# Kernel tuning notes

Hardware: AMD Instinct MI355X
Metric: run time of the kernel (lower is better)

## Reference

```python
import jax, jax.numpy as jnp
import numpy as np

NUM_SONGS = 2000
N1 = NUM_SONGS + 1  # incl. padding idx 0
EMB = 64
B = 32
S = 5    # num_prev_shows
M = 25   # max_songs_per_show


def setup_inputs() -> dict:
    key = jax.random.key(0)
    ks = jax.random.split(key, 32)
    def lin(k, i, o):
        kw, kb = jax.random.split(k)
        s = 1.0 / np.sqrt(i)
        return (jax.random.uniform(kw, (i, o), jnp.float32, -s, s),
                jax.random.uniform(kb, (o,), jnp.float32, -s, s))
    song_emb = jax.random.normal(ks[0], (N1, EMB), jnp.float32)
    song_emb = song_emb.at[0].set(0.0)  # padding_idx=0
    gcn_w1, gcn_b1 = lin(ks[1], EMB, EMB)
    gcn_w2, gcn_b2 = lin(ks[2], EMB, EMB)
    q_w, q_b = lin(ks[3], EMB, EMB)
    k_w, k_b = lin(ks[4], EMB, EMB)
    v_w, v_b = lin(ks[5], EMB, EMB)
    venue_t = jax.random.normal(ks[6], (200, EMB // 4), jnp.float32)
    tour_t = jax.random.normal(ks[7], (20, EMB // 4), jnp.float32)
    country_t = jax.random.normal(ks[8], (50, EMB // 8), jnp.float32)
    fest_t = jax.random.normal(ks[9], (2, EMB // 8), jnp.float32)
    mara_t = jax.random.normal(ks[10], (2, EMB // 8), jnp.float32)
    ctx_in = EMB // 2 + 3 * (EMB // 8)  # 56
    ctx_w, ctx_b = lin(ks[11], ctx_in, EMB)
    p1_w, p1_b = lin(ks[12], EMB * 3, EMB * 2)
    p2_w, p2_b = lin(ks[13], EMB * 2, EMB)
    p3_w, p3_b = lin(ks[14], EMB, 1)
    return {
        'song_ids': jax.random.randint(ks[20], (B,), 0, N1),
        'prev_setlists': jax.random.randint(ks[21], (B, S, M), 0, N1),
        'venue_ids': jax.random.randint(ks[22], (B,), 0, 200),
        'tour_ids': jax.random.randint(ks[23], (B,), 0, 20),
        'country_ids': jax.random.randint(ks[24], (B,), 0, 50),
        'is_festival': jax.random.randint(ks[25], (B,), 0, 2),
        'is_marathon': jax.random.randint(ks[26], (B,), 0, 2),
        'song_emb': song_emb,
        'gcn_w1': gcn_w1, 'gcn_b1': gcn_b1, 'gcn_w2': gcn_w2, 'gcn_b2': gcn_b2,
        'q_w': q_w, 'q_b': q_b, 'k_w': k_w, 'k_b': k_b, 'v_w': v_w, 'v_b': v_b,
        'venue_t': venue_t, 'tour_t': tour_t, 'country_t': country_t,
        'fest_t': fest_t, 'mara_t': mara_t,
        'ctx_w': ctx_w, 'ctx_b': ctx_b,
        'p1_w': p1_w, 'p1_b': p1_b, 'p2_w': p2_w, 'p2_b': p2_b,
        'p3_w': p3_w, 'p3_b': p3_b,
    }


def _build_adj(prev_setlists):
    # co-occurrence counts via one scatter-add (replaces nested python loops)
    b, s, m = prev_setlists.shape
    mask = prev_setlists > 0
    pair_ok = (mask[:, :, :, None] & mask[:, :, None, :]
               & ~jnp.eye(m, dtype=bool))  # exclude same position i==j
    flat_idx = (prev_setlists[:, :, :, None] * N1
                + prev_setlists[:, :, None, :]).reshape(b, -1)
    w = pair_ok.astype(jnp.float32).reshape(b, -1)
    adj = jnp.zeros((b, N1 * N1), jnp.float32)
    adj = adj.at[jnp.arange(b)[:, None], flat_idx].add(w)
    adj = adj.reshape(b, N1, N1)
    return adj / (adj.sum(axis=2, keepdims=True) + 1e-10)


def _forward(song_ids, prev_setlists, venue_ids, tour_ids, country_ids,
             is_festival, is_marathon, song_emb, gcn_w1, gcn_b1, gcn_w2,
             gcn_b2, q_w, q_b, k_w, k_b, v_w, v_b, venue_t, tour_t,
             country_t, fest_t, mara_t, ctx_w, ctx_b, p1_w, p1_b, p2_w,
             p2_b, p3_w, p3_b):
    b = song_ids.shape[0]
    adj = _build_adj(prev_setlists)                      # [B,N1,N1]
    x = jnp.broadcast_to(song_emb[None], (b, N1, EMB))   # [B,N1,E]
    for w_, b_ in ((gcn_w1, gcn_b1), (gcn_w2, gcn_b2)):
        agg = jnp.einsum('bnm,bme->bne', adj, x)
        x = jax.nn.relu(agg @ w_ + b_)
    song_embs = x
    # ragged masked-mean show embeddings
    mask = (prev_setlists > 0).astype(jnp.float32)       # [B,S,M]
    gathered = jax.vmap(lambda se, ids: se[ids])(song_embs, prev_setlists)  # [B,S,M,E]
    cnt = mask.sum(-1, keepdims=True)                    # [B,S,1]
    show_embs = jnp.where(cnt > 0,
                          (gathered * mask[..., None]).sum(2) / jnp.maximum(cnt, 1.0),
                          0.0)                           # [B,S,E]
    ctx = jnp.concatenate([venue_t[venue_ids], tour_t[tour_ids],
                           country_t[country_ids], fest_t[is_festival],
                           mara_t[is_marathon]], axis=-1)
    ctx = ctx @ ctx_w + ctx_b                            # [B,E]
    # temporal attention
    q = ctx @ q_w + q_b                                  # [B,E]
    k = show_embs @ k_w + k_b                            # [B,S,E]
    v = show_embs @ v_w + v_b
    scores = jnp.einsum('be,bse->bs', q, k) / jnp.sqrt(jnp.float32(EMB))
    attn = jax.nn.softmax(scores, axis=-1)
    attended = jnp.einsum('bs,bse->be', attn, v)
    cand = song_embs[jnp.arange(b), song_ids]
    h = jnp.concatenate([cand, ctx, attended], axis=-1)  # [B,3E]
    h = jax.nn.relu(h @ p1_w + p1_b)   # dropout is eval-mode identity
    h = jax.nn.relu(h @ p2_w + p2_b)
    logits = (h @ p3_w + p3_b).squeeze(-1)
    return jax.nn.sigmoid(logits)


def reference(song_ids, prev_setlists, venue_ids, tour_ids, country_ids,
              is_festival, is_marathon, song_emb, gcn_w1, gcn_b1, gcn_w2,
              gcn_b2, q_w, q_b, k_w, k_b, v_w, v_b, venue_t, tour_t,
              country_t, fest_t, mara_t, ctx_w, ctx_b, p1_w, p1_b, p2_w,
              p2_b, p3_w, p3_b):
    return _forward(song_ids, prev_setlists, venue_ids, tour_ids,
                    country_ids, is_festival, is_marathon, song_emb,
                    gcn_w1, gcn_b1, gcn_w2, gcn_b2, q_w, q_b, k_w, k_b,
                    v_w, v_b, venue_t, tour_t, country_t, fest_t, mara_t,
                    ctx_w, ctx_b, p1_w, p1_b, p2_w, p2_b, p3_w, p3_b)
```

## Files before the change

### kernel.cpp

```cpp
#include <hip/hip_runtime.h>

#define N1    2001
#define EMB   64
#define NSHOW 5
#define MSONG 25
#define NPOS  (NSHOW * MSONG)
#define MAXU  128
#define NT    1024
#define WT    68

__global__ __launch_bounds__(NT)
__attribute__((amdgpu_waves_per_eu(4, 4)))
void setsgnn_kernel(
    const int* __restrict__ song_ids,
    const int* __restrict__ prev_setlists,
    const int* __restrict__ venue_ids,
    const int* __restrict__ tour_ids,
    const int* __restrict__ country_ids,
    const int* __restrict__ is_festival,
    const int* __restrict__ is_marathon,
    const float* __restrict__ song_emb,
    const float* __restrict__ gcn_w1, const float* __restrict__ gcn_b1,
    const float* __restrict__ gcn_w2, const float* __restrict__ gcn_b2,
    const float* __restrict__ q_w,  const float* __restrict__ q_b,
    const float* __restrict__ k_w,  const float* __restrict__ k_b,
    const float* __restrict__ v_w,  const float* __restrict__ v_b,
    const float* __restrict__ venue_t, const float* __restrict__ tour_t,
    const float* __restrict__ country_t, const float* __restrict__ fest_t,
    const float* __restrict__ mara_t,
    const float* __restrict__ ctx_w, const float* __restrict__ ctx_b,
    const float* __restrict__ p1_w,  const float* __restrict__ p1_b,
    const float* __restrict__ p2_w,  const float* __restrict__ p2_b,
    const float* __restrict__ p3_w,  const float* __restrict__ p3_b,
    float* __restrict__ out)
{
    const int b    = blockIdx.x;
    const int tid  = threadIdx.x;
    const int wv   = tid >> 6;
    const int lane = tid & 63;
    const int col0 = tid & 63;
    const int eq0  = tid >> 6;

    __shared__ __align__(16) float xb0[MAXU][EMB];
    __shared__ __align__(16) float wldsT[2][EMB][WT];
    __shared__ __align__(16) float ctxw_l[56][EMB];
    __shared__ __align__(16) float qw_l[EMB][EMB];
    __shared__ __align__(16) float blds[2][EMB];
    __shared__ __align__(16) float bias_ctx[EMB], bias_q[EMB], bias_k[EMB], bias_v[EMB];
    __shared__ __align__(16) float bias_p1[128], bias_p2[EMB], bias_p3w[EMB];
    __shared__ float bias_p3b;
    __shared__ unsigned short idmap[N1];
    __shared__ int   sl[NPOS];
    __shared__ int   pmap[NPOS];
    __shared__ int   list_ids[MAXU];
    __shared__ float c_us[MAXU][NSHOW];
    __shared__ float occv[MAXU];
    __shared__ float invv[MAXU];
    __shared__ float cntm1[NSHOW];
    __shared__ float invc[NSHOW];
    __shared__ int   U_cnt;
    __shared__ __align__(16) float Xsum[NSHOW][EMB];
    __shared__ float XW[NSHOW][EMB];
    __shared__ float ctxin[56];
    __shared__ float ctxv[EMB];
    __shared__ float qv[EMB];
    __shared__ float vatt[NSHOW][EMB];
    __shared__ float attnw[NSHOW];
    __shared__ float hbuf[3 * EMB];
    __shared__ float h1b[128];
    __shared__ float partial[NT];

    float w1r[4], w2r[4];
    #pragma unroll
    for (int j = 0; j < 4; j++) w1r[j] = gcn_w1[(eq0 * 4 + j) * EMB + col0];
    #pragma unroll
    for (int j = 0; j < 4; j++) w2r[j] = gcn_w2[(eq0 * 4 + j) * EMB + col0];
    const float4 qw4 = ((const float4*)q_w)[tid];
    float4 cw4 = make_float4(0.f, 0.f, 0.f, 0.f);
    if (tid < 896) cw4 = ((const float4*)ctx_w)[tid];
    float4 bb;
    if (tid < 32) bb = (tid < 16) ? ((const float4*)gcn_b1)[tid]
                                  : ((const float4*)gcn_b2)[tid - 16];
    const int slr = (tid < NPOS) ? prev_setlists[b * NPOS + tid] : 0;
    const int sid    = song_ids[b];
    const int vid    = venue_ids[b];
    const int tourid = tour_ids[b];
    const int cid    = country_ids[b];
    const int fid    = is_festival[b];
    const int mid    = is_marathon[b];

    for (int i = tid; i < N1; i += NT) idmap[i] = 0xFFFFu;
    if (tid < MAXU * NSHOW) ((float*)c_us)[tid] = 0.f;
    if (tid < NPOS) sl[tid] = slr;
    if (tid == 0) U_cnt = 0;
    *(float4*)&wldsT[0][col0][eq0 * 4] = make_float4(w1r[0], w1r[1], w1r[2], w1r[3]);
    *(float4*)&wldsT[1][col0][eq0 * 4] = make_float4(w2r[0], w2r[1], w2r[2], w2r[3]);
    ((float4*)qw_l)[tid] = qw4;
    if (tid < 896) ((float4*)ctxw_l)[tid] = cw4;
    if (tid < 32) ((float4*)blds)[tid] = bb;
    {
        int r = tid - 256;
        if (r >= 0 && r < 16)        ((float4*)bias_ctx)[r]       = ((const float4*)ctx_b)[r];
        else if (r >= 16 && r < 32)  ((float4*)bias_q)[r - 16]    = ((const float4*)q_b)[r - 16];
        else if (r >= 32 && r < 48)  ((float4*)bias_k)[r - 32]    = ((const float4*)k_b)[r - 32];
        else if (r >= 48 && r < 64)  ((float4*)bias_v)[r - 48]    = ((const float4*)v_b)[r - 48];
        else if (r >= 64 && r < 96)  ((float4*)bias_p1)[r - 64]   = ((const float4*)p1_b)[r - 64];
        else if (r >= 96 && r < 112) ((float4*)bias_p2)[r - 96]   = ((const float4*)p2_b)[r - 96];
        else if (r >= 112 && r < 128)((float4*)bias_p3w)[r - 112] = ((const float4*)p3_w)[r - 112];
        else if (r == 128)           bias_p3b = p3_b[0];
    }
    __syncthreads();

    if (tid < NPOS) { int id = sl[tid]; if (id > 0) idmap[id] = 1u; }
    if (tid == NPOS) idmap[sid] = 1u;
    if (tid >= 128 && tid < 128 + NSHOW) {
        int s = tid - 128, c = 0;
        for (int i = 0; i < MSONG; i++) c += (sl[s * MSONG + i] > 0) ? 1 : 0;
        cntm1[s] = (float)(c - 1);
        invc[s] = 1.f / fmaxf((float)c, 1.f);
    }
    if (tid >= 144 && tid < 200) {
        int e = tid - 144; float val;
        if (e < 16)      val = venue_t[vid * 16 + e];
        else if (e < 32) val = tour_t[tourid * 16 + (e - 16)];
        else if (e < 40) val = country_t[cid * 8 + (e - 32)];
        else if (e < 48) val = fest_t[fid * 8 + (e - 40)];
        else             val = mara_t[mid * 8 + (e - 48)];
        ctxin[e] = val;
    }
    __syncthreads();

    for (int i = tid; i < N1; i += NT) {
        const bool p = (idmap[i] == 1u);
        const unsigned long long m = __ballot(p);
        int base = 0;
        if (lane == 0) { int c = __popcll(m); if (c) base = atomicAdd(&U_cnt, c); }
        base = __shfl(base, 0, 64);
        if (p) {
            int r = __popcll(m & ((1ull << lane) - 1ull));
            int u = base + r;
            idmap[i] = (unsigned short)u;
            list_ids[u] = i;
        }
    }
    __syncthreads();
    const int U = U_cnt;

    if (tid < NPOS) {
        int id = sl[tid];
        int pm = (id > 0) ? (int)idmap[id] : -1;
        pmap[tid] = pm;
        if (pm >= 0) atomicAdd(&c_us[pm][tid / MSONG], 1.f);
    }
    if (tid >= 896 && tid < 960) {
        int c = tid - 896;
        float acc = bias_ctx[c];
        #pragma unroll
        for (int e = 0; e < 56; e++) acc += ctxin[e] * ctxw_l[e][c];
        ctxv[c] = acc;
    }
    for (int t = tid; t < MAXU * (EMB / 4); t += NT) {
        int u = t >> 4, e4 = t & 15;
        float4 v = make_float4(0.f, 0.f, 0.f, 0.f);
        if (u < U) v = ((const float4*)(song_emb + list_ids[u] * EMB))[e4];
        *(float4*)&xb0[u][e4 * 4] = v;
    }
    __syncthreads();

    if (tid < MAXU) {
        float o = 0.f, r = 0.f;
        #pragma unroll
        for (int s = 0; s < NSHOW; s++) { float cc = c_us[tid][s]; o += cc; r += cc * cntm1[s]; }
        occv[tid] = o; invv[tid] = 1.f / (r + 1e-10f);
    }
    if (tid >= 128 && tid < 192) {
        int c = tid - 128;
        float acc = bias_q[c];
        #pragma unroll
        for (int e = 0; e < EMB; e++) acc += ctxv[e] * qw_l[e][c];
        qv[c] = acc;
    }
    if (wv >= 6 && wv < 11) {
        int s = wv - 6;
        int pm[MSONG];
        #pragma unroll
        for (int i = 0; i < MSONG; i++) pm[i] = pmap[s * MSONG + i];
        float acc = 0.f;
        #pragma unroll
        for (int i = 0; i < MSONG; i++) if (pm[i] >= 0) acc += xb0[pm[i]][lane];
        Xsum[s][lane] = acc;
    }
    __syncthreads();

    if (tid < NSHOW * EMB) {
        int s = tid >> 6, c = tid & 63;
        float acc = 0.f;
        #pragma unroll 4
        for (int e4 = 0; e4 < 16; e4++) {
            const float4 w4 = *(const float4*)&wldsT[0][c][e4 * 4];
            const float4 xs = *(const float4*)&Xsum[s][e4 * 4];
            acc += w4.x * xs.x + w4.y * xs.y + w4.z * xs.z + w4.w * xs.w;
        }
        XW[s][c] = acc;
    }
    __syncthreads();

    #define GCN_BODY(L)                                                          \
    {                                                                            \
        const float bias = blds[L][lane];                                        \
        float y[8];                                                              \
        _Pragma("unroll")                                                        \
        for (int uu = 0; uu < 8; ++uu) y[uu] = 0.f;                              \
        _Pragma("unroll 4")                                                      \
        for (int e4 = 0; e4 < 16; ++e4) {                                        \
            float4 a[8];                                                         \
            _Pragma("unroll")                                                    \
            for (int uu = 0; uu < 8; ++uu)                                       \
                a[uu] = *(const float4*)&xb0[(uu << 4) | wv][e4 * 4];            \
            const float4 w4 = *(const float4*)&wldsT[L][lane][e4 * 4];           \
            _Pragma("unroll")                                                    \
            for (int uu = 0; uu < 8; ++uu)                                       \
                y[uu] += a[uu].x * w4.x + a[uu].y * w4.y                         \
                       + a[uu].z * w4.z + a[uu].w * w4.w;                        \
        }                                                                        \
        _Pragma("unroll")                                                        \
        for (int uu = 0; uu < 8; ++uu) {                                         \
            const int u = (uu << 4) | wv;                                        \
            float acc = c_us[u][0] * XW[0][lane] + c_us[u][1] * XW[1][lane]      \
                      + c_us[u][2] * XW[2][lane] + c_us[u][3] * XW[3][lane]      \
                      + c_us[u][4] * XW[4][lane];                                \
            float val = (acc - occv[u] * y[uu]) * invv[u] + bias;                \
            xb0[u][lane] = fmaxf(val, 0.f);                                      \
        }                                                                        \
    }

    GCN_BODY(0)
    __syncthreads();

    {
        float kr[4];
        #pragma unroll
        for (int j = 0; j < 4; j++) kr[j] = k_w[(eq0 * 4 + j) * EMB + col0];
        if (wv >= 6 && wv < 11) {
            int s = wv - 6;
            int pm[MSONG];
            #pragma unroll
            for (int i = 0; i < MSONG; i++) pm[i] = pmap[s * MSONG + i];
            float acc = 0.f;
            #pragma unroll
            for (int i = 0; i < MSONG; i++) if (pm[i] >= 0) acc += xb0[pm[i]][lane];
            Xsum[s][lane] = acc;
        }
        *(float4*)&wldsT[0][col0][eq0 * 4] = make_float4(kr[0], kr[1], kr[2], kr[3]);
    }
    __syncthreads();

    if (tid < NSHOW * EMB) {
        int s = tid >> 6, c = tid & 63;
        float acc = 0.f;
        #pragma unroll 4
        for (int e4 = 0; e4 < 16; e4++) {
            const float4 w4 = *(const float4*)&wldsT[1][c][e4 * 4];
            const float4 xs = *(const float4*)&Xsum[s][e4 * 4];
            acc += w4.x * xs.x + w4.y * xs.y + w4.z * xs.z + w4.w * xs.w;
        }
        XW[s][c] = acc;
    }
    __syncthreads();

    float vr[4];
    #pragma unroll
    for (int j = 0; j < 4; j++) vr[j] = v_w[(eq0 * 4 + j) * EMB + col0];
    GCN_BODY(1)
    __syncthreads();

    *(float4*)&wldsT[1][col0][eq0 * 4] = make_float4(vr[0], vr[1], vr[2], vr[3]);
    const int kk1 = tid >> 7, o1 = tid & 127;
    const int kk2 = tid >> 6, o2 = lane;
    float p1wr[24], p2wr[8];
    #pragma unroll
    for (int j = 0; j < 24; j++) p1wr[j] = p1_w[(kk1 * 24 + j) * 128 + o1];
    #pragma unroll
    for (int j = 0; j < 8; j++)  p2wr[j] = p2_w[(kk2 * 8 + j) * 64 + o2];

    if (wv >= 6 && wv < 11) {
        int s = wv - 6;
        int pm[MSONG];
        #pragma unroll
        for (int i = 0; i < MSONG; i++) pm[i] = pmap[s * MSONG + i];
        float acc = 0.f;
        #pragma unroll
        for (int i = 0; i < MSONG; i++) if (pm[i] >= 0) acc += xb0[pm[i]][lane];
        Xsum[s][lane] = acc;
    }
    if (tid < 64)                    hbuf[tid] = xb0[(int)idmap[sid]][tid];
    else if (tid >= 64 && tid < 128) hbuf[tid] = ctxv[tid - 64];
    __syncthreads();

    if (wv < NSHOW) {
        float s0 = 0.f;
        #pragma unroll 4
        for (int e4 = 0; e4 < 16; e4++) {
            const float4 w4 = *(const float4*)&wldsT[0][lane][e4 * 4];
            const float4 xs = *(const float4*)&Xsum[wv][e4 * 4];
            s0 += w4.x * xs.x + w4.y * xs.y + w4.z * xs.z + w4.w * xs.w;
        }
        float kk = s0 * invc[wv] + bias_k[lane];
        float p = kk * qv[lane];
        #pragma unroll
        for (int o = 32; o > 0; o >>= 1) p += __shfl_xor(p, o, 64);
        if (lane == 0) attnw[wv] = p * 0.125f;
    }
    if (wv >= 5 && wv < 10) {
        int s = wv - 5;
        float s0 = 0.f;
        #pragma unroll 4
        for (int e4 = 0; e4 < 16; e4++) {
            const float4 w4 = *(const float4*)&wldsT[1][lane][e4 * 4];
            const float4 xs = *(const float4*)&Xsum[s][e4 * 4];
            s0 += w4.x * xs.x + w4.y * xs.y + w4.z * xs.z + w4.w * xs.w;
        }
        vatt[s][lane] = s0 * invc[s] + bias_v[lane];
    }
    __syncthreads();

    if (wv == 0) {
        float a0 = attnw[0], a1 = attnw[1], a2 = attnw[2], a3 = attnw[3], a4 = attnw[4];
        float mx = fmaxf(fmaxf(fmaxf(a0, a1), fmaxf(a2, a3)), a4);
        float e0 = expf(a0 - mx), e1 = expf(a1 - mx), e2 = expf(a2 - mx),
              e3 = expf(a3 - mx), e4 = expf(a4 - mx);
        float isum = 1.f / (e0 + e1 + e2 + e3 + e4);
        float att = (e0 * vatt[0][lane] + e1 * vatt[1][lane] + e2 * vatt[2][lane]
                   + e3 * vatt[3][lane] + e4 * vatt[4][lane]) * isum;
        hbuf[2 * EMB + lane] = att;
    }
    __syncthreads();

    {
        float acc = (kk1 == 0) ? bias_p1[o1] : 0.f;
        #pragma unroll
        for (int j = 0; j < 24; j++) acc += hbuf[kk1 * 24 + j] * p1wr[j];
        partial[tid] = acc;
    }
    __syncthreads();

    if (tid < 128) {
        float acc = 0.f;
        #pragma unroll
        for (int kk = 0; kk < 8; kk++) acc += partial[kk * 128 + tid];
        h1b[tid] = fmaxf(acc, 0.f);
    }
    __syncthreads();

    {
        float acc = (kk2 == 0) ? bias_p2[o2] : 0.f;
        #pragma unroll
        for (int j = 0; j < 8; j++) acc += h1b[kk2 * 8 + j] * p2wr[j];
        partial[tid] = acc;
    }
    __syncthreads();

    if (wv == 0) {
        float acc = 0.f;
        #pragma unroll
        for (int kk = 0; kk < 16; kk++) acc += partial[kk * 64 + lane];
        float h2 = fmaxf(acc, 0.f);
        float p = h2 * bias_p3w[lane];
        #pragma unroll
        for (int o = 32; o > 0; o >>= 1) p += __shfl_xor(p, o, 64);
        if (lane == 0) out[b] = 1.f / (1.f + expf(-(p + bias_p3b)));
    }
}

extern "C" void kernel_launch(void* const* d_in, const int* in_sizes, int n_in,
                              void* d_out, int out_size, void* d_ws, size_t ws_size,
                              hipStream_t stream) {
    (void)n_in; (void)out_size; (void)d_ws; (void)ws_size;
    const int B = in_sizes[0];
    setsgnn_kernel<<<B, NT, 0, stream>>>(
        (const int*)d_in[0], (const int*)d_in[1], (const int*)d_in[2],
        (const int*)d_in[3], (const int*)d_in[4], (const int*)d_in[5],
        (const int*)d_in[6],
        (const float*)d_in[7],
        (const float*)d_in[8],  (const float*)d_in[9],
        (const float*)d_in[10], (const float*)d_in[11],
        (const float*)d_in[12], (const float*)d_in[13],
        (const float*)d_in[14], (const float*)d_in[15],
        (const float*)d_in[16], (const float*)d_in[17],
        (const float*)d_in[18], (const float*)d_in[19],
        (const float*)d_in[20], (const float*)d_in[21],
        (const float*)d_in[22],
        (const float*)d_in[23], (const float*)d_in[24],
        (const float*)d_in[25], (const float*)d_in[26],
        (const float*)d_in[27], (const float*)d_in[28],
        (const float*)d_in[29], (const float*)d_in[30],
        (float*)d_out);
}
```

Baseline: 32.73 us.

## Reassociate GCN aggregation to sum transformed rows and fuse attention into MLP

```diff
diff --git a/kernel.cpp b/kernel.cpp
--- a/kernel.cpp
+++ b/kernel.cpp
@@ -42,6 +42,7 @@
     const int eq0  = tid >> 6;
 
     __shared__ __align__(16) float xb0[MAXU][EMB];
+    __shared__ __align__(16) float ybuf[MAXU][EMB];
     __shared__ __align__(16) float wldsT[2][EMB][WT];
     __shared__ __align__(16) float ctxw_l[56][EMB];
     __shared__ __align__(16) float qw_l[EMB][EMB];
@@ -66,7 +67,6 @@
     __shared__ float qv[EMB];
     __shared__ float vatt[NSHOW][EMB];
     __shared__ float attnw[NSHOW];
-    __shared__ float hbuf[3 * EMB];
     __shared__ float h1b[128];
     __shared__ float partial[NT];
 
@@ -143,15 +143,6 @@
             list_ids[u] = i;
         }
     }
-    __syncthreads();
-    const int U = U_cnt;
-
-    if (tid < NPOS) {
-        int id = sl[tid];
-        int pm = (id > 0) ? (int)idmap[id] : -1;
-        pmap[tid] = pm;
-        if (pm >= 0) atomicAdd(&c_us[pm][tid / MSONG], 1.f);
-    }
     if (tid >= 896 && tid < 960) {
         int c = tid - 896;
         float acc = bias_ctx[c];
@@ -159,56 +150,11 @@
         for (int e = 0; e < 56; e++) acc += ctxin[e] * ctxw_l[e][c];
         ctxv[c] = acc;
     }
-    for (int t = tid; t < MAXU * (EMB / 4); t += NT) {
-        int u = t >> 4, e4 = t & 15;
-        float4 v = make_float4(0.f, 0.f, 0.f, 0.f);
-        if (u < U) v = ((const float4*)(song_emb + list_ids[u] * EMB))[e4];
-        *(float4*)&xb0[u][e4 * 4] = v;
-    }
-    __syncthreads();
-
-    if (tid < MAXU) {
-        float o = 0.f, r = 0.f;
-        #pragma unroll
-        for (int s = 0; s < NSHOW; s++) { float cc = c_us[tid][s]; o += cc; r += cc * cntm1[s]; }
-        occv[tid] = o; invv[tid] = 1.f / (r + 1e-10f);
-    }
-    if (tid >= 128 && tid < 192) {
-        int c = tid - 128;
-        float acc = bias_q[c];
-        #pragma unroll
-        for (int e = 0; e < EMB; e++) acc += ctxv[e] * qw_l[e][c];
-        qv[c] = acc;
-    }
-    if (wv >= 6 && wv < 11) {
-        int s = wv - 6;
-        int pm[MSONG];
-        #pragma unroll
-        for (int i = 0; i < MSONG; i++) pm[i] = pmap[s * MSONG + i];
-        float acc = 0.f;
-        #pragma unroll
-        for (int i = 0; i < MSONG; i++) if (pm[i] >= 0) acc += xb0[pm[i]][lane];
-        Xsum[s][lane] = acc;
-    }
-    __syncthreads();
-
-    if (tid < NSHOW * EMB) {
-        int s = tid >> 6, c = tid & 63;
-        float acc = 0.f;
-        #pragma unroll 4
-        for (int e4 = 0; e4 < 16; e4++) {
-            const float4 w4 = *(const float4*)&wldsT[0][c][e4 * 4];
-            const float4 xs = *(const float4*)&Xsum[s][e4 * 4];
-            acc += w4.x * xs.x + w4.y * xs.y + w4.z * xs.z + w4.w * xs.w;
-        }
-        XW[s][c] = acc;
-    }
-    __syncthreads();
-
-    #define GCN_BODY(L)                                                          \
+    __syncthreads();
+    const int U = U_cnt;
+
+    #define Y_COMPUTE(L)                                                         \
     {                                                                            \
-        const float bias = blds[L][lane];                                        \
-        float y[8];                                                              \
         _Pragma("unroll")                                                        \
         for (int uu = 0; uu < 8; ++uu) y[uu] = 0.f;                              \
         _Pragma("unroll 4")                                                      \
@@ -224,6 +170,12 @@
                        + a[uu].z * w4.z + a[uu].w * w4.w;                        \
         }                                                                        \
         _Pragma("unroll")                                                        \
+        for (int uu = 0; uu < 8; ++uu) ybuf[(uu << 4) | wv][lane] = y[uu];       \
+    }
+    #define COMBINE(L)                                                           \
+    {                                                                            \
+        const float bias = blds[L][lane];                                        \
+        _Pragma("unroll")                                                        \
         for (int uu = 0; uu < 8; ++uu) {                                         \
             const int u = (uu << 4) | wv;                                        \
             float acc = c_us[u][0] * XW[0][lane] + c_us[u][1] * XW[1][lane]      \
@@ -234,47 +186,75 @@
         }                                                                        \
     }
 
-    GCN_BODY(0)
+    float y[8];
+    if (tid < NPOS) {
+        int id = sl[tid];
+        int pm = (id > 0) ? (int)idmap[id] : -1;
+        pmap[tid] = pm;
+        if (pm >= 0) atomicAdd(&c_us[pm][tid / MSONG], 1.f);
+    }
+    if (tid >= 128 && tid < 192) {
+        int c = tid - 128;
+        float acc = bias_q[c];
+        #pragma unroll
+        for (int e = 0; e < EMB; e++) acc += ctxv[e] * qw_l[e][c];
+        qv[c] = acc;
+    }
+    #pragma unroll
+    for (int g = 0; g < 2; ++g) {
+        const int uu = g * 4 + (lane >> 4);
+        const int u  = (uu << 4) | wv;
+        const int e4 = lane & 15;
+        float4 v = make_float4(0.f, 0.f, 0.f, 0.f);
+        if (u < U) v = ((const float4*)(song_emb + list_ids[u] * EMB))[e4];
+        *(float4*)&xb0[u][e4 * 4] = v;
+    }
+    Y_COMPUTE(0)
     __syncthreads();
 
     {
         float kr[4];
         #pragma unroll
         for (int j = 0; j < 4; j++) kr[j] = k_w[(eq0 * 4 + j) * EMB + col0];
-        if (wv >= 6 && wv < 11) {
-            int s = wv - 6;
-            int pm[MSONG];
-            #pragma unroll
-            for (int i = 0; i < MSONG; i++) pm[i] = pmap[s * MSONG + i];
+        if (wv < NSHOW) {
             float acc = 0.f;
             #pragma unroll
-            for (int i = 0; i < MSONG; i++) if (pm[i] >= 0) acc += xb0[pm[i]][lane];
-            Xsum[s][lane] = acc;
+            for (int i = 0; i < MSONG; i++) {
+                int pm = pmap[wv * MSONG + i];
+                if (pm >= 0) acc += ybuf[pm][lane];
+            }
+            XW[wv][lane] = acc;
+        }
+        if (tid >= 320 && tid < 448) {
+            int u = tid - 320;
+            float o = 0.f, r = 0.f;
+            #pragma unroll
+            for (int s = 0; s < NSHOW; s++) { float cc = c_us[u][s]; o += cc; r += cc * cntm1[s]; }
+            occv[u] = o; invv[u] = 1.f / (r + 1e-10f);
         }
         *(float4*)&wldsT[0][col0][eq0 * 4] = make_float4(kr[0], kr[1], kr[2], kr[3]);
     }
     __syncthreads();
 
-    if (tid < NSHOW * EMB) {
-        int s = tid >> 6, c = tid & 63;
+    float vr[4];
+    #pragma unroll
+    for (int j = 0; j < 4; j++) vr[j] = v_w[(eq0 * 4 + j) * EMB + col0];
+    COMBINE(0)
+    Y_COMPUTE(1)
+    __syncthreads();
+
+    if (wv < NSHOW) {
         float acc = 0.f;
-        #pragma unroll 4
-        for (int e4 = 0; e4 < 16; e4++) {
-            const float4 w4 = *(const float4*)&wldsT[1][c][e4 * 4];
-            const float4 xs = *(const float4*)&Xsum[s][e4 * 4];
-            acc += w4.x * xs.x + w4.y * xs.y + w4.z * xs.z + w4.w * xs.w;
-        }
-        XW[s][c] = acc;
-    }
-    __syncthreads();
-
-    float vr[4];
-    #pragma unroll
-    for (int j = 0; j < 4; j++) vr[j] = v_w[(eq0 * 4 + j) * EMB + col0];
-    GCN_BODY(1)
-    __syncthreads();
-
+        #pragma unroll
+        for (int i = 0; i < MSONG; i++) {
+            int pm = pmap[wv * MSONG + i];
+            if (pm >= 0) acc += ybuf[pm][lane];
+        }
+        XW[wv][lane] = acc;
+    }
     *(float4*)&wldsT[1][col0][eq0 * 4] = make_float4(vr[0], vr[1], vr[2], vr[3]);
+    __syncthreads();
+
     const int kk1 = tid >> 7, o1 = tid & 127;
     const int kk2 = tid >> 6, o2 = lane;
     float p1wr[24], p2wr[8];
@@ -282,6 +262,8 @@
     for (int j = 0; j < 24; j++) p1wr[j] = p1_w[(kk1 * 24 + j) * 128 + o1];
     #pragma unroll
     for (int j = 0; j < 8; j++)  p2wr[j] = p2_w[(kk2 * 8 + j) * 64 + o2];
+    COMBINE(1)
+    __syncthreads();
 
     if (wv >= 6 && wv < 11) {
         int s = wv - 6;
@@ -293,8 +275,6 @@
         for (int i = 0; i < MSONG; i++) if (pm[i] >= 0) acc += xb0[pm[i]][lane];
         Xsum[s][lane] = acc;
     }
-    if (tid < 64)                    hbuf[tid] = xb0[(int)idmap[sid]][tid];
-    else if (tid >= 64 && tid < 128) hbuf[tid] = ctxv[tid - 64];
     __syncthreads();
 
     if (wv < NSHOW) {
@@ -324,22 +304,27 @@
     }
     __syncthreads();
 
-    if (wv == 0) {
+    {
         float a0 = attnw[0], a1 = attnw[1], a2 = attnw[2], a3 = attnw[3], a4 = attnw[4];
         float mx = fmaxf(fmaxf(fmaxf(a0, a1), fmaxf(a2, a3)), a4);
-        float e0 = expf(a0 - mx), e1 = expf(a1 - mx), e2 = expf(a2 - mx),
-              e3 = expf(a3 - mx), e4 = expf(a4 - mx);
-        float isum = 1.f / (e0 + e1 + e2 + e3 + e4);
-        float att = (e0 * vatt[0][lane] + e1 * vatt[1][lane] + e2 * vatt[2][lane]
-                   + e3 * vatt[3][lane] + e4 * vatt[4][lane]) * isum;
-        hbuf[2 * EMB + lane] = att;
-    }
-    __syncthreads();
-
-    {
+        float ex0 = expf(a0 - mx), ex1 = expf(a1 - mx), ex2 = expf(a2 - mx),
+              ex3 = expf(a3 - mx), ex4 = expf(a4 - mx);
+        float isum = 1.f / (ex0 + ex1 + ex2 + ex3 + ex4);
+        const int uc = (int)idmap[sid];
         float acc = (kk1 == 0) ? bias_p1[o1] : 0.f;
         #pragma unroll
-        for (int j = 0; j < 24; j++) acc += hbuf[kk1 * 24 + j] * p1wr[j];
+        for (int j = 0; j < 24; j++) {
+            int e = kk1 * 24 + j;
+            float h;
+            if (e < 64)       h = xb0[uc][e];
+            else if (e < 128) h = ctxv[e - 64];
+            else {
+                int d = e - 128;
+                h = (ex0 * vatt[0][d] + ex1 * vatt[1][d] + ex2 * vatt[2][d]
+                   + ex3 * vatt[3][d] + ex4 * vatt[4][d]) * isum;
+            }
+            acc += h * p1wr[j];
+        }
         partial[tid] = acc;
     }
     __syncthreads();
```

Result: slower. 35.07 us (+7.2%).

## Preload all four 64x64 weights into LDS upfront and loop the GCN layers

Applied to the files above, without the earlier changes.

```diff
diff --git a/kernel.cpp b/kernel.cpp
--- a/kernel.cpp
+++ b/kernel.cpp
@@ -42,7 +42,7 @@
     const int eq0  = tid >> 6;
 
     __shared__ __align__(16) float xb0[MAXU][EMB];
-    __shared__ __align__(16) float wldsT[2][EMB][WT];
+    __shared__ __align__(16) float wldsT[4][EMB][WT];
     __shared__ __align__(16) float ctxw_l[56][EMB];
     __shared__ __align__(16) float qw_l[EMB][EMB];
     __shared__ __align__(16) float blds[2][EMB];
@@ -70,17 +70,23 @@
     __shared__ float h1b[128];
     __shared__ float partial[NT];
 
-    float w1r[4], w2r[4];
-    #pragma unroll
-    for (int j = 0; j < 4; j++) w1r[j] = gcn_w1[(eq0 * 4 + j) * EMB + col0];
-    #pragma unroll
-    for (int j = 0; j < 4; j++) w2r[j] = gcn_w2[(eq0 * 4 + j) * EMB + col0];
-    const float4 qw4 = ((const float4*)q_w)[tid];
-    float4 cw4 = make_float4(0.f, 0.f, 0.f, 0.f);
-    if (tid < 896) cw4 = ((const float4*)ctx_w)[tid];
-    float4 bb;
-    if (tid < 32) bb = (tid < 16) ? ((const float4*)gcn_b1)[tid]
-                                  : ((const float4*)gcn_b2)[tid - 16];
+    {
+        const float* wps[4] = { gcn_w1, gcn_w2, k_w, v_w };
+        float wr[4][4];
+        #pragma unroll
+        for (int m = 0; m < 4; m++)
+            #pragma unroll
+            for (int j = 0; j < 4; j++) wr[m][j] = wps[m][(eq0 * 4 + j) * EMB + col0];
+        #pragma unroll
+        for (int m = 0; m < 4; m++)
+            *(float4*)&wldsT[m][col0][eq0 * 4] = make_float4(wr[m][0], wr[m][1], wr[m][2], wr[m][3]);
+    }
+    ((float4*)qw_l)[tid] = ((const float4*)q_w)[tid];
+    if (tid < 896) ((float4*)ctxw_l)[tid] = ((const float4*)ctx_w)[tid];
+    if (tid < 32) {
+        float4 bb = (tid < 16) ? ((const float4*)gcn_b1)[tid] : ((const float4*)gcn_b2)[tid - 16];
+        ((float4*)blds)[tid] = bb;
+    }
     const int slr = (tid < NPOS) ? prev_setlists[b * NPOS + tid] : 0;
     const int sid    = song_ids[b];
     const int vid    = venue_ids[b];
@@ -93,11 +99,6 @@
     if (tid < MAXU * NSHOW) ((float*)c_us)[tid] = 0.f;
     if (tid < NPOS) sl[tid] = slr;
     if (tid == 0) U_cnt = 0;
-    *(float4*)&wldsT[0][col0][eq0 * 4] = make_float4(w1r[0], w1r[1], w1r[2], w1r[3]);
-    *(float4*)&wldsT[1][col0][eq0 * 4] = make_float4(w2r[0], w2r[1], w2r[2], w2r[3]);
-    ((float4*)qw_l)[tid] = qw4;
-    if (tid < 896) ((float4*)ctxw_l)[tid] = cw4;
-    if (tid < 32) ((float4*)blds)[tid] = bb;
     {
         int r = tid - 256;
         if (r >= 0 && r < 16)        ((float4*)bias_ctx)[r]       = ((const float4*)ctx_b)[r];
@@ -155,7 +156,7 @@
     if (tid >= 896 && tid < 960) {
         int c = tid - 896;
         float acc = bias_ctx[c];
-        #pragma unroll
+        #pragma unroll 2
         for (int e = 0; e < 56; e++) acc += ctxin[e] * ctxw_l[e][c];
         ctxv[c] = acc;
     }
@@ -176,105 +177,70 @@
     if (tid >= 128 && tid < 192) {
         int c = tid - 128;
         float acc = bias_q[c];
-        #pragma unroll
+        #pragma unroll 2
         for (int e = 0; e < EMB; e++) acc += ctxv[e] * qw_l[e][c];
         qv[c] = acc;
     }
     if (wv >= 6 && wv < 11) {
         int s = wv - 6;
-        int pm[MSONG];
-        #pragma unroll
-        for (int i = 0; i < MSONG; i++) pm[i] = pmap[s * MSONG + i];
         float acc = 0.f;
         #pragma unroll
-        for (int i = 0; i < MSONG; i++) if (pm[i] >= 0) acc += xb0[pm[i]][lane];
+        for (int i = 0; i < MSONG; i++) { int pm = pmap[s * MSONG + i]; if (pm >= 0) acc += xb0[pm][lane]; }
         Xsum[s][lane] = acc;
     }
     __syncthreads();
 
-    if (tid < NSHOW * EMB) {
-        int s = tid >> 6, c = tid & 63;
-        float acc = 0.f;
-        #pragma unroll 4
-        for (int e4 = 0; e4 < 16; e4++) {
-            const float4 w4 = *(const float4*)&wldsT[0][c][e4 * 4];
-            const float4 xs = *(const float4*)&Xsum[s][e4 * 4];
-            acc += w4.x * xs.x + w4.y * xs.y + w4.z * xs.z + w4.w * xs.w;
-        }
-        XW[s][c] = acc;
-    }
-    __syncthreads();
-
-    #define GCN_BODY(L)                                                          \
-    {                                                                            \
-        const float bias = blds[L][lane];                                        \
-        float y[8];                                                              \
-        _Pragma("unroll")                                                        \
-        for (int uu = 0; uu < 8; ++uu) y[uu] = 0.f;                              \
-        _Pragma("unroll 4")                                                      \
-        for (int e4 = 0; e4 < 16; ++e4) {                                        \
-            float4 a[8];                                                         \
-            _Pragma("unroll")                                                    \
-            for (int uu = 0; uu < 8; ++uu)                                       \
-                a[uu] = *(const float4*)&xb0[(uu << 4) | wv][e4 * 4];            \
-            const float4 w4 = *(const float4*)&wldsT[L][lane][e4 * 4];           \
-            _Pragma("unroll")                                                    \
-            for (int uu = 0; uu < 8; ++uu)                                       \
-                y[uu] += a[uu].x * w4.x + a[uu].y * w4.y                         \
-                       + a[uu].z * w4.z + a[uu].w * w4.w;                        \
-        }                                                                        \
-        _Pragma("unroll")                                                        \
-        for (int uu = 0; uu < 8; ++uu) {                                         \
-            const int u = (uu << 4) | wv;                                        \
-            float acc = c_us[u][0] * XW[0][lane] + c_us[u][1] * XW[1][lane]      \
-                      + c_us[u][2] * XW[2][lane] + c_us[u][3] * XW[3][lane]      \
-                      + c_us[u][4] * XW[4][lane];                                \
-            float val = (acc - occv[u] * y[uu]) * invv[u] + bias;                \
-            xb0[u][lane] = fmaxf(val, 0.f);                                      \
-        }                                                                        \
-    }
-
-    GCN_BODY(0)
-    __syncthreads();
-
-    {
-        float kr[4];
-        #pragma unroll
-        for (int j = 0; j < 4; j++) kr[j] = k_w[(eq0 * 4 + j) * EMB + col0];
+    for (int l = 0; l < 2; ++l) {
+        if (wv < NSHOW) {
+            float acc = 0.f;
+            #pragma unroll 2
+            for (int e4 = 0; e4 < 16; e4++) {
+                const float4 w4 = *(const float4*)&wldsT[l][lane][e4 * 4];
+                const float4 xs = *(const float4*)&Xsum[wv][e4 * 4];
+                acc += w4.x * xs.x + w4.y * xs.y + w4.z * xs.z + w4.w * xs.w;
+            }
+            XW[wv][lane] = acc;
+        }
+        __syncthreads();
+
+        {
+            const float bias = blds[l][lane];
+            float y[8];
+            #pragma unroll
+            for (int uu = 0; uu < 8; ++uu) y[uu] = 0.f;
+            #pragma unroll 2
+            for (int e4 = 0; e4 < 16; ++e4) {
+                float4 a[8];
+                #pragma unroll
+                for (int uu = 0; uu < 8; ++uu)
+                    a[uu] = *(const float4*)&xb0[(uu << 4) | wv][e4 * 4];
+                const float4 w4 = *(const float4*)&wldsT[l][lane][e4 * 4];
+                #pragma unroll
+                for (int uu = 0; uu < 8; ++uu)
+                    y[uu] += a[uu].x * w4.x + a[uu].y * w4.y + a[uu].z * w4.z + a[uu].w * w4.w;
+            }
+            #pragma unroll
+            for (int uu = 0; uu < 8; ++uu) {
+                const int u = (uu << 4) | wv;
+                float acc = c_us[u][0] * XW[0][lane] + c_us[u][1] * XW[1][lane]
+                          + c_us[u][2] * XW[2][lane] + c_us[u][3] * XW[3][lane]
+                          + c_us[u][4] * XW[4][lane];
+                float val = (acc - occv[u] * y[uu]) * invv[u] + bias;
+                xb0[u][lane] = fmaxf(val, 0.f);
+            }
+        }
+        __syncthreads();
+
         if (wv >= 6 && wv < 11) {
             int s = wv - 6;
-            int pm[MSONG];
-            #pragma unroll
-            for (int i = 0; i < MSONG; i++) pm[i] = pmap[s * MSONG + i];
             float acc = 0.f;
             #pragma unroll
-            for (int i = 0; i < MSONG; i++) if (pm[i] >= 0) acc += xb0[pm[i]][lane];
+            for (int i = 0; i < MSONG; i++) { int pm = pmap[s * MSONG + i]; if (pm >= 0) acc += xb0[pm][lane]; }
             Xsum[s][lane] = acc;
         }
-        *(float4*)&wldsT[0][col0][eq0 * 4] = make_float4(kr[0], kr[1], kr[2], kr[3]);
-    }
-    __syncthreads();
-
-    if (tid < NSHOW * EMB) {
-        int s = tid >> 6, c = tid & 63;
-        float acc = 0.f;
-        #pragma unroll 4
-        for (int e4 = 0; e4 < 16; e4++) {
-            const float4 w4 = *(const float4*)&wldsT[1][c][e4 * 4];
-            const float4 xs = *(const float4*)&Xsum[s][e4 * 4];
-            acc += w4.x * xs.x + w4.y * xs.y + w4.z * xs.z + w4.w * xs.w;
-        }
-        XW[s][c] = acc;
-    }
-    __syncthreads();
-
-    float vr[4];
-    #pragma unroll
-    for (int j = 0; j < 4; j++) vr[j] = v_w[(eq0 * 4 + j) * EMB + col0];
-    GCN_BODY(1)
-    __syncthreads();
-
-    *(float4*)&wldsT[1][col0][eq0 * 4] = make_float4(vr[0], vr[1], vr[2], vr[3]);
+        __syncthreads();
+    }
+
     const int kk1 = tid >> 7, o1 = tid & 127;
     const int kk2 = tid >> 6, o2 = lane;
     float p1wr[24], p2wr[8];
@@ -283,25 +249,11 @@
     #pragma unroll
     for (int j = 0; j < 8; j++)  p2wr[j] = p2_w[(kk2 * 8 + j) * 64 + o2];
 
-    if (wv >= 6 && wv < 11) {
-        int s = wv - 6;
-        int pm[MSONG];
-        #pragma unroll
-        for (int i = 0; i < MSONG; i++) pm[i] = pmap[s * MSONG + i];
-        float acc = 0.f;
-        #pragma unroll
-        for (int i = 0; i < MSONG; i++) if (pm[i] >= 0) acc += xb0[pm[i]][lane];
-        Xsum[s][lane] = acc;
-    }
-    if (tid < 64)                    hbuf[tid] = xb0[(int)idmap[sid]][tid];
-    else if (tid >= 64 && tid < 128) hbuf[tid] = ctxv[tid - 64];
-    __syncthreads();
-
     if (wv < NSHOW) {
         float s0 = 0.f;
-        #pragma unroll 4
+        #pragma unroll 2
         for (int e4 = 0; e4 < 16; e4++) {
-            const float4 w4 = *(const float4*)&wldsT[0][lane][e4 * 4];
+            const float4 w4 = *(const float4*)&wldsT[2][lane][e4 * 4];
             const float4 xs = *(const float4*)&Xsum[wv][e4 * 4];
             s0 += w4.x * xs.x + w4.y * xs.y + w4.z * xs.z + w4.w * xs.w;
         }
@@ -314,14 +266,16 @@
     if (wv >= 5 && wv < 10) {
         int s = wv - 5;
         float s0 = 0.f;
-        #pragma unroll 4
+        #pragma unroll 2
         for (int e4 = 0; e4 < 16; e4++) {
-            const float4 w4 = *(const float4*)&wldsT[1][lane][e4 * 4];
+            const float4 w4 = *(const float4*)&wldsT[3][lane][e4 * 4];
             const float4 xs = *(const float4*)&Xsum[s][e4 * 4];
             s0 += w4.x * xs.x + w4.y * xs.y + w4.z * xs.z + w4.w * xs.w;
         }
         vatt[s][lane] = s0 * invc[s] + bias_v[lane];
     }
+    if (tid >= 640 && tid < 704)       hbuf[tid - 640] = xb0[(int)idmap[sid]][tid - 640];
+    else if (tid >= 704 && tid < 768)  hbuf[64 + (tid - 704)] = ctxv[tid - 704];
     __syncthreads();
 
     if (wv == 0) {
```

Measured after the change: 35.17 us. +7.4%, slower.
